# Performance work log

Measured on AMD Instinct MI355X. Metric: run time of the kernel, lower is better.

Reference implementation:

```python
import jax, jax.numpy as jnp
import numpy as np

# static config (matches torch module instantiation)
B, D, NH, HD = 2, 256, 8, 32
NL, NP, DFF = 1, 4, 1024
SHAPES = [(180, 180)]          # (H, W) per level; 180*180 = 32400
STARTS = [0]
LSRC = 32400
N_DET, N_SEG = 200, 100        # SEG_QUERY_NUM=100 -> num_seg_query=300
LQ = N_DET + N_SEG


def _lin(key, dout, din, scale=None):
    scale = scale if scale is not None else 1.0 / np.sqrt(din)
    k1, k2 = jax.random.split(key)
    return (jax.random.normal(k1, (dout, din), jnp.float32) * scale,
            jax.random.normal(k2, (dout,), jnp.float32) * 0.01)


def setup_inputs() -> dict:
    key = jax.random.key(0)
    ks = iter(jax.random.split(key, 64))
    inp = {
        'query': jax.random.normal(next(ks), (B, LQ, D), jnp.float32),
        'query_pos': jax.random.normal(next(ks), (B, LQ, D), jnp.float32),
        'src': jax.random.normal(next(ks), (B, LSRC, D), jnp.float32),
        'pos': jax.random.normal(next(ks), (B, LSRC, D), jnp.float32),
        'reference_points': jax.random.uniform(next(ks), (B, LSRC + LQ, NL, 2), jnp.float32),
        'spatial_shapes': jnp.array(SHAPES, jnp.int32),
        'level_start_index': jnp.array(STARTS, jnp.int32),
    }
    # two MSDeformAttn instances (self_attn = sa_*, cross_attn = ca_*)
    for pre in ('sa', 'ca'):
        inp[pre + '_Wv'], inp[pre + '_bv'] = _lin(next(ks), D, D)
        inp[pre + '_Woff'], inp[pre + '_boff'] = _lin(next(ks), NH * NL * NP * 2, D, scale=0.01)
        inp[pre + '_Waw'], inp[pre + '_baw'] = _lin(next(ks), NH * NL * NP, D, scale=0.01)
        inp[pre + '_Wout'], inp[pre + '_bout'] = _lin(next(ks), D, D)
    for nm in ('norm1', 'norm2', 'normq', 'qa_norm', 'norm3'):
        inp[nm + '_g'] = jnp.ones((D,), jnp.float32)
        inp[nm + '_b'] = jnp.zeros((D,), jnp.float32)
    inp['ffn1_W1'], inp['ffn1_b1'] = _lin(next(ks), DFF, D)
    inp['ffn1_W2'], inp['ffn1_b2'] = _lin(next(ks), D, DFF)
    inp['ffn3_W1'], inp['ffn3_b1'] = _lin(next(ks), DFF, D)
    inp['ffn3_W2'], inp['ffn3_b2'] = _lin(next(ks), D, DFF)
    # TCSLayer: proj(d->2d) then gate1/gate2 (d->d), sigmoid gates
    inp['tcs_Wp'], inp['tcs_bp'] = _lin(next(ks), 2 * D, D)
    inp['tcs_Wg1'], inp['tcs_bg1'] = _lin(next(ks), D, D)
    inp['tcs_Wg2'], inp['tcs_bg2'] = _lin(next(ks), D, D)
    # query self-attention (nn.MultiheadAttention): packed in_proj [3D, D]
    inp['qa_Win'], inp['qa_bin'] = _lin(next(ks), 3 * D, D)
    inp['qa_Wout'], inp['qa_bout'] = _lin(next(ks), D, D)
    return inp


def ln(x, g, b, eps=1e-5):
    m = x.mean(-1, keepdims=True)
    v = ((x - m) ** 2).mean(-1, keepdims=True)
    return (x - m) * jax.lax.rsqrt(v + eps) * g + b


def msda(q, ref, src_v, Wv, bv, Woff, boff, Waw, baw, Wout, bout):
    """MSDeformAttn: value proj -> learned offsets/weights -> bilinear sample -> out proj.
    q [B,Lq,D], ref [B,Lq,NL,2] in [0,1], src_v [B,Lin,D]."""
    Bq, Lq, _ = q.shape
    Lin = src_v.shape[1]
    value = (src_v @ Wv.T + bv).reshape(Bq, Lin, NH, HD).transpose(0, 2, 1, 3)  # [B,NH,Lin,HD]
    off = (q @ Woff.T + boff).reshape(Bq, Lq, NH, NL, NP, 2)
    aw = jax.nn.softmax((q @ Waw.T + baw).reshape(Bq, Lq, NH, NL * NP), -1)
    aw = aw.reshape(Bq, Lq, NH, NL, NP)
    norm = jnp.array([[w, h] for (h, w) in SHAPES], q.dtype)  # [NL,2] = (W,H)
    loc = ref[:, :, None, :, None, :] + off / norm[None, None, None, :, None, :]
    out = jnp.zeros((Bq, NH, Lq, HD), q.dtype)
    for l, (h, w) in enumerate(SHAPES):
        s = STARTS[l]
        v_l = value[:, :, s:s + h * w, :]
        # grid_sample align_corners=False: pixel = loc*size - 0.5, zero padding
        x = loc[:, :, :, l, :, 0] * w - 0.5  # [B,Lq,NH,NP]
        y = loc[:, :, :, l, :, 1] * h - 0.5
        x0 = jnp.floor(x); y0 = jnp.floor(y)
        lx = x - x0; ly = y - y0
        x0i = x0.astype(jnp.int32); y0i = y0.astype(jnp.int32)
        samp = jnp.zeros((Bq, NH, Lq, NP, HD), q.dtype)
        for dy, dx, wgt in ((0, 0, (1 - lx) * (1 - ly)), (0, 1, lx * (1 - ly)),
                            (1, 0, (1 - lx) * ly), (1, 1, lx * ly)):
            xi = x0i + dx; yi = y0i + dy
            valid = ((xi >= 0) & (xi < w) & (yi >= 0) & (yi < h)).astype(q.dtype)
            idx = jnp.clip(yi, 0, h - 1) * w + jnp.clip(xi, 0, w - 1)  # [B,Lq,NH,NP]
            idx_t = idx.transpose(0, 2, 1, 3).reshape(Bq, NH, Lq * NP)
            g = jnp.take_along_axis(v_l, idx_t[..., None], axis=2).reshape(Bq, NH, Lq, NP, HD)
            samp = samp + g * (wgt * valid).transpose(0, 2, 1, 3)[..., None]
        out = out + jnp.einsum('bhqpd,bqhp->bhqd', samp, aw[:, :, :, l, :])
    out = out.transpose(0, 2, 1, 3).reshape(Bq, Lq, NH * HD)
    return out @ Wout.T + bout


def mha(x, pos, Win, bin_, Wout, bout):
    qk = x + pos
    q = (qk @ Win[:D].T + bin_[:D]).reshape(*x.shape[:2], NH, HD)
    k = (qk @ Win[D:2 * D].T + bin_[D:2 * D]).reshape(*x.shape[:2], NH, HD)
    v = (x @ Win[2 * D:].T + bin_[2 * D:]).reshape(*x.shape[:2], NH, HD)
    attn = jax.nn.softmax(jnp.einsum('bqhd,bkhd->bhqk', q, k) / np.sqrt(HD), -1)
    o = jnp.einsum('bhqk,bkhd->bqhd', attn, v).reshape(*x.shape[:2], D)
    return o @ Wout.T + bout


def reference(query, query_pos, src, pos, reference_points, spatial_shapes, level_start_index,
              sa_Wv, sa_bv, sa_Woff, sa_boff, sa_Waw, sa_baw, sa_Wout, sa_bout,
              ca_Wv, ca_bv, ca_Woff, ca_boff, ca_Waw, ca_baw, ca_Wout, ca_bout,
              norm1_g, norm1_b, norm2_g, norm2_b, normq_g, normq_b,
              qa_norm_g, qa_norm_b, norm3_g, norm3_b,
              ffn1_W1, ffn1_b1, ffn1_W2, ffn1_b2,
              ffn3_W1, ffn3_b1, ffn3_W2, ffn3_b2,
              tcs_Wp, tcs_bp, tcs_Wg1, tcs_bg1, tcs_Wg2, tcs_bg2,
              qa_Win, qa_bin, qa_Wout, qa_bout):
    # deformable self-attn over BEV tokens
    src2 = msda(src + pos, reference_points[:, :LSRC], src,
                sa_Wv, sa_bv, sa_Woff, sa_boff, sa_Waw, sa_baw, sa_Wout, sa_bout)
    src = ln(src + src2, norm1_g, norm1_b)
    # FFN 1
    h = jax.nn.relu(src @ ffn1_W1.T + ffn1_b1) @ ffn1_W2.T + ffn1_b2
    src = ln(src + h, norm2_g, norm2_b)
    # TCS gating (USE_SIGMOID_GATE, not SPLIT_GATE, no OCC)
    gd, gs = jnp.split(jax.nn.gelu(src @ tcs_Wp.T + tcs_bp, approximate=False), 2, axis=-1)
    gate_det = jax.nn.sigmoid(gd @ tcs_Wg1.T + tcs_bg1)
    gate_seg = jax.nn.sigmoid(gs @ tcs_Wg2.T + tcs_bg2)
    # gated deformable cross-attn (shared cross_attn weights)
    q_det = msda(query[:, :N_DET] + query_pos[:, :N_DET],
                 reference_points[:, LSRC:LSRC + N_DET], src * gate_det,
                 ca_Wv, ca_bv, ca_Woff, ca_boff, ca_Waw, ca_baw, ca_Wout, ca_bout)
    q_seg = msda(query[:, N_DET:LQ] + query_pos[:, N_DET:LQ],
                 reference_points[:, LSRC + N_DET:LSRC + LQ], src * gate_seg,
                 ca_Wv, ca_bv, ca_Woff, ca_boff, ca_Waw, ca_baw, ca_Wout, ca_bout)
    query2 = jnp.concatenate([q_det, q_seg], 1)
    query = ln(query + query2, normq_g, normq_b)
    # query self-attention (post-norm)
    query = ln(query + mha(query, query_pos, qa_Win, qa_bin, qa_Wout, qa_bout),
               qa_norm_g, qa_norm_b)
    # FFN 3
    h3 = jax.nn.relu(query @ ffn3_W1.T + ffn3_b1) @ ffn3_W2.T + ffn3_b2
    query = ln(query + h3, norm3_g, norm3_b)
    return (query, src, gate_det, gate_seg)
```

## Files before the change

### kernel.cpp

```cpp
#include <hip/hip_runtime.h>
#include <hip/hip_bf16.h>
#include <cmath>

using bf16 = __hip_bfloat16;
typedef __bf16 bf16x8 __attribute__((ext_vector_type(8)));
typedef __bf16 bf16x4 __attribute__((ext_vector_type(4)));
typedef float f32x4 __attribute__((ext_vector_type(4)));

constexpr int D = 256;
constexpr int LSRC = 32400;
constexpr int NB = 2;
constexpr int LQ = 300;
constexpr int NDET = 200;
constexpr int MS = NB * LSRC;
constexpr int MQ = NB * LQ;
constexpr int RP_STRIDE = LSRC + LQ;
constexpr float IMGW = 180.f, IMGH = 180.f;
constexpr int IW = 180, IH = 180;

constexpr long long OFF_Q  = 0;
constexpr long long OFF_S  = (long long)MQ * D;
constexpr long long OFF_GD = OFF_S + (long long)MS * D;
constexpr long long OFF_GS = OFF_GD + (long long)MS * D;

__device__ inline void gload16(const void* g, void* l) {
  __builtin_amdgcn_global_load_lds(
      (const __attribute__((address_space(1))) void*)g,
      (__attribute__((address_space(3))) void*)l, 16, 0, 0);
}

__global__ void detect_kernel(const void* g, int* flag) {
  *flag = (*(const unsigned*)g == 0x3F803F80u) ? 1 : 0;
}

struct CvtEnt { const void* src; void* dst; int n; int f32out; };
struct CvtBatch { CvtEnt e[48]; int blk0[49]; int cnt; };

__global__ __launch_bounds__(256) void cvt_batch_kernel(CvtBatch cb, const int* __restrict__ flag) {
  int bid = blockIdx.x;
  int i = 0;
  for (int j = 1; j < cb.cnt; ++j) if (cb.blk0[j] <= bid) i = j;
  const CvtEnt en = cb.e[i];
  int idx = (bid - cb.blk0[i]) * 2048 + threadIdx.x * 8;
  if (idx >= en.n) return;
  const bool isb = (*flag != 0);
  if (en.f32out) {
    float v[8];
    if (isb) {
      bf16x8 x = *(const bf16x8*)((const __bf16*)en.src + idx);
#pragma unroll
      for (int j = 0; j < 8; ++j) v[j] = (float)x[j];
    } else {
      const float* s = (const float*)en.src + idx;
#pragma unroll
      for (int j = 0; j < 8; ++j) v[j] = s[j];
    }
    float* o = (float*)en.dst + idx;
#pragma unroll
    for (int j = 0; j < 8; ++j) o[j] = v[j];
  } else {
    if (isb) {
      uint4 x = *(const uint4*)((const char*)en.src + (size_t)idx * 2);
      *(uint4*)((char*)en.dst + (size_t)idx * 2) = x;
    } else {
      const float* s = (const float*)en.src + idx;
      bf16x8 o;
#pragma unroll
      for (int j = 0; j < 8; ++j) o[j] = (__bf16)s[j];
      *(bf16x8*)((__bf16*)en.dst + idx) = o;
    }
  }
}

__global__ __launch_bounds__(256) void cvt_add(const void* __restrict__ a, const void* __restrict__ b,
                                               const int* __restrict__ flag,
                                               bf16* __restrict__ a_b, bf16* __restrict__ b_b,
                                               bf16* __restrict__ sum, int n8) {
  int i = blockIdx.x * 256 + threadIdx.x;
  if (i >= n8) return;
  const bool isb = (*flag != 0);
  float va[8], vb[8];
  bf16x8 ab, bb;
  if (isb) {
    ab = *(const bf16x8*)((const __bf16*)a + (size_t)i * 8);
    bb = *(const bf16x8*)((const __bf16*)b + (size_t)i * 8);
#pragma unroll
    for (int j = 0; j < 8; ++j) { va[j] = (float)ab[j]; vb[j] = (float)bb[j]; }
  } else {
    const float* pa = (const float*)a + (size_t)i * 8;
    const float* pb = (const float*)b + (size_t)i * 8;
#pragma unroll
    for (int j = 0; j < 8; ++j) { va[j] = pa[j]; vb[j] = pb[j]; ab[j] = (__bf16)va[j]; bb[j] = (__bf16)vb[j]; }
  }
  bf16x8 sb;
#pragma unroll
  for (int j = 0; j < 8; ++j) sb[j] = (__bf16)(va[j] + vb[j]);
  if (a_b) *(bf16x8*)((__bf16*)a_b + (size_t)i * 8) = ab;
  if (b_b) *(bf16x8*)((__bf16*)b_b + (size_t)i * 8) = bb;
  *(bf16x8*)((__bf16*)sum + (size_t)i * 8) = sb;
}

__global__ __launch_bounds__(256) void add8(const bf16* __restrict__ a, const bf16* __restrict__ b,
                                            bf16* __restrict__ o, int n8) {
  int i = blockIdx.x * 256 + threadIdx.x;
  if (i >= n8) return;
  bf16x8 va = *(const bf16x8*)((const __bf16*)a + (size_t)i * 8);
  bf16x8 vb = *(const bf16x8*)((const __bf16*)b + (size_t)i * 8);
  bf16x8 vo;
#pragma unroll
  for (int j = 0; j < 8; ++j) vo[j] = (__bf16)((float)va[j] + (float)vb[j]);
  *(bf16x8*)((__bf16*)o + (size_t)i * 8) = vo;
}

template<int ACT, int OUTB, int RESM>
__global__ __launch_bounds__(256) void gemm_bt(
    const bf16* __restrict__ A, int lda,
    const bf16* __restrict__ Wt,
    const bf16* __restrict__ bias,
    const void* __restrict__ res,
    void* __restrict__ out, int ldo,
    int M, int N, int K)
{
  __shared__ __bf16 As[64 * 32];
  __shared__ __bf16 Bs[64 * 32];
  const int m0 = blockIdx.x * 64;
  const int n0 = blockIdx.y * 64;
  const int tid = threadIdx.x;
  const int lane = tid & 63, wid = tid >> 6;
  const int wm = (wid >> 1) * 32, wn = (wid & 1) * 32;
  f32x4 acc[2][2] = {};
  const int lr = tid >> 2;
  const int lc = (tid & 3) * 8;
  const bf16* Ap = A + (size_t)(m0 + lr) * lda + lc;
  const bf16* Wp = Wt + (size_t)(n0 + lr) * K + lc;
  __bf16* AsP = &As[8 * tid];
  __bf16* BsP = &Bs[8 * tid];
  const int fr = lane & 15, ks = (lane >> 4) * 8;

  for (int k0 = 0; k0 < K; k0 += 32) {
    __syncthreads();
    gload16((const __bf16*)Ap + k0, AsP);
    gload16((const __bf16*)Wp + k0, BsP);
    __syncthreads();
    bf16x8 a0 = *(const bf16x8*)&As[(wm + fr) * 32 + ks];
    bf16x8 a1 = *(const bf16x8*)&As[(wm + 16 + fr) * 32 + ks];
    bf16x8 b0 = *(const bf16x8*)&Bs[(wn + fr) * 32 + ks];
    bf16x8 b1 = *(const bf16x8*)&Bs[(wn + 16 + fr) * 32 + ks];
    acc[0][0] = __builtin_amdgcn_mfma_f32_16x16x32_bf16(a0, b0, acc[0][0], 0, 0, 0);
    acc[0][1] = __builtin_amdgcn_mfma_f32_16x16x32_bf16(a0, b1, acc[0][1], 0, 0, 0);
    acc[1][0] = __builtin_amdgcn_mfma_f32_16x16x32_bf16(a1, b0, acc[1][0], 0, 0, 0);
    acc[1][1] = __builtin_amdgcn_mfma_f32_16x16x32_bf16(a1, b1, acc[1][1], 0, 0, 0);
  }

  const int rq = (lane >> 4) * 4;
#pragma unroll
  for (int fm = 0; fm < 2; ++fm)
#pragma unroll
  for (int fn = 0; fn < 2; ++fn) {
    int ncol = n0 + wn + fn * 16 + fr;
    if (ncol >= N) continue;
    float bvs = (float)bias[ncol];
#pragma unroll
    for (int i = 0; i < 4; ++i) {
      int mrow = m0 + wm + fm * 16 + rq + i;
      if (mrow >= M) continue;
      float v = acc[fm][fn][i] + bvs;
      if (RESM == 1) v += (float)((const bf16*)res)[(size_t)mrow * ldo + ncol];
      else if (RESM == 2) v += ((const float*)res)[(size_t)mrow * ldo + ncol];
      if (ACT == 1) v = fmaxf(v, 0.f);
      else if (ACT == 2) v = 0.5f * v * (1.f + erff(v * 0.7071067811865476f));
      else if (ACT == 3) v = 1.f / (1.f + __expf(-v));
      if (OUTB) ((bf16*)out)[(size_t)mrow * ldo + ncol] = (bf16)v;
      else ((float*)out)[(size_t)mrow * ldo + ncol] = v;
    }
  }
}

template<int ACT, int OUTB, int RESM, int EMIT>
__global__ __launch_bounds__(256) void gemm128(
    const bf16* __restrict__ A, int lda,
    const bf16* __restrict__ Wt,
    const bf16* __restrict__ bias,
    const void* __restrict__ res,
    void* __restrict__ out, int ldo,
    int M, int N, int K,
    const int* __restrict__ flagp, void* __restrict__ ob, long long eoff)
{
  __shared__ __bf16 As[128 * 32];
  __shared__ __bf16 Bs[128 * 32];
  const int m0 = blockIdx.x * 128;
  const int n0 = blockIdx.y * 128;
  const int tid = threadIdx.x;
  const int lane = tid & 63, wid = tid >> 6;
  const int wr = (wid >> 1) * 64, wc = (wid & 1) * 64;
  const int fr = lane & 15, ks = (lane >> 4) * 8;
  f32x4 acc[4][4] = {};

  const int srow = tid >> 2;
  const int scol = (tid & 3) * 8;
  const bf16* Ap0 = A + (size_t)(m0 + srow) * lda + scol;
  const bf16* Ap1 = A + (size_t)(m0 + 64 + srow) * lda + scol;
  const bf16* Bp0 = Wt + (size_t)(n0 + srow) * K + scol;
  const bf16* Bp1 = Wt + (size_t)(n0 + 64 + srow) * K + scol;
  __bf16* AsP0 = &As[8 * tid];
  __bf16* AsP1 = &As[64 * 32 + 8 * tid];
  __bf16* BsP0 = &Bs[8 * tid];
  __bf16* BsP1 = &Bs[64 * 32 + 8 * tid];

  for (int k0 = 0; k0 < K; k0 += 32) {
    __syncthreads();
    gload16((const __bf16*)Ap0 + k0, AsP0);
    gload16((const __bf16*)Ap1 + k0, AsP1);
    gload16((const __bf16*)Bp0 + k0, BsP0);
    gload16((const __bf16*)Bp1 + k0, BsP1);
    __syncthreads();
    bf16x8 af[4], bfv[4];
#pragma unroll
    for (int m = 0; m < 4; ++m) af[m]  = *(const bf16x8*)&As[(wr + m * 16 + fr) * 32 + ks];
#pragma unroll
    for (int n = 0; n < 4; ++n) bfv[n] = *(const bf16x8*)&Bs[(wc + n * 16 + fr) * 32 + ks];
#pragma unroll
    for (int m = 0; m < 4; ++m)
#pragma unroll
      for (int n = 0; n < 4; ++n)
        acc[m][n] = __builtin_amdgcn_mfma_f32_16x16x32_bf16(af[m], bfv[n], acc[m][n], 0, 0, 0);
  }

  const bool isb = EMIT ? (*flagp != 0) : false;
  const int rq = (lane >> 4) * 4;
#pragma unroll
  for (int m = 0; m < 4; ++m) {
    const int mb = m0 + wr + m * 16 + rq;
#pragma unroll
    for (int n = 0; n < 4; ++n) {
      const int ncol = n0 + wc + n * 16 + fr;
      const float bvs = (float)bias[ncol];
#pragma unroll
      for (int i = 0; i < 4; ++i) {
        const int mrow = mb + i;
        if (mrow >= M) continue;
        float v = acc[m][n][i] + bvs;
        if (RESM == 1) v += (float)((const bf16*)res)[(size_t)mrow * ldo + ncol];
        else if (RESM == 2) v += ((const float*)res)[(size_t)mrow * ldo + ncol];
        if (ACT == 1) v = fmaxf(v, 0.f);
        else if (ACT == 2) v = 0.5f * v * (1.f + erff(v * 0.7071067811865476f));
        else if (ACT == 3) v = 1.f / (1.f + __expf(-v));
        if (OUTB) ((bf16*)out)[(size_t)mrow * ldo + ncol] = (bf16)v;
        else ((float*)out)[(size_t)mrow * ldo + ncol] = v;
        if (EMIT) {
          long long eo = eoff + (long long)mrow * ldo + ncol;
          if (isb) ((__bf16*)ob)[eo] = (__bf16)v;
          else ((float*)ob)[eo] = v;
        }
      }
    }
  }
}

__global__ __launch_bounds__(256) void gemm_gated(
    const bf16* __restrict__ S, const bf16* __restrict__ G, int lda,
    const bf16* __restrict__ Wt,
    const bf16* __restrict__ bias,
    bf16* __restrict__ out, int ldo,
    int M, int N, int K)
{
  __shared__ __bf16 As[128 * 32];
  __shared__ __bf16 Bs[128 * 32];
  const int m0 = blockIdx.x * 128;
  const int n0 = blockIdx.y * 128;
  const int tid = threadIdx.x;
  const int lane = tid & 63, wid = tid >> 6;
  const int wr = (wid >> 1) * 64, wc = (wid & 1) * 64;
  const int fr = lane & 15, ks = (lane >> 4) * 8;
  f32x4 acc[4][4] = {};

  const int srow = tid >> 2;
  const int scol = (tid & 3) * 8;
  const bf16* Sp0 = S + (size_t)(m0 + srow) * lda + scol;
  const bf16* Sp1 = S + (size_t)(m0 + 64 + srow) * lda + scol;
  const bf16* Gp0 = G + (size_t)(m0 + srow) * lda + scol;
  const bf16* Gp1 = G + (size_t)(m0 + 64 + srow) * lda + scol;
  const bf16* Bp0 = Wt + (size_t)(n0 + srow) * K + scol;
  const bf16* Bp1 = Wt + (size_t)(n0 + 64 + srow) * K + scol;
  __bf16* AsP0 = &As[8 * tid];
  __bf16* AsP1 = &As[64 * 32 + 8 * tid];

  for (int k0 = 0; k0 < K; k0 += 32) {
    bf16x8 s0 = *(const bf16x8*)((const __bf16*)Sp0 + k0);
    bf16x8 g0 = *(const bf16x8*)((const __bf16*)Gp0 + k0);
    bf16x8 s1 = *(const bf16x8*)((const __bf16*)Sp1 + k0);
    bf16x8 g1 = *(const bf16x8*)((const __bf16*)Gp1 + k0);
    bf16x8 a0, a1;
#pragma unroll
    for (int j = 0; j < 8; ++j) {
      a0[j] = (__bf16)((float)s0[j] * (float)g0[j]);
      a1[j] = (__bf16)((float)s1[j] * (float)g1[j]);
    }
    __syncthreads();
    *(bf16x8*)AsP0 = a0;
    *(bf16x8*)AsP1 = a1;
    gload16((const __bf16*)Bp0 + k0, &Bs[8 * tid]);
    gload16((const __bf16*)Bp1 + k0, &Bs[64 * 32 + 8 * tid]);
    __syncthreads();
    bf16x8 af[4], bfv[4];
#pragma unroll
    for (int m = 0; m < 4; ++m) af[m]  = *(const bf16x8*)&As[(wr + m * 16 + fr) * 32 + ks];
#pragma unroll
    for (int n = 0; n < 4; ++n) bfv[n] = *(const bf16x8*)&Bs[(wc + n * 16 + fr) * 32 + ks];
#pragma unroll
    for (int m = 0; m < 4; ++m)
#pragma unroll
      for (int n = 0; n < 4; ++n)
        acc[m][n] = __builtin_amdgcn_mfma_f32_16x16x32_bf16(af[m], bfv[n], acc[m][n], 0, 0, 0);
  }

  const int rq = (lane >> 4) * 4;
#pragma unroll
  for (int m = 0; m < 4; ++m) {
    const int mb = m0 + wr + m * 16 + rq;
#pragma unroll
    for (int n = 0; n < 4; ++n) {
      const int ncol = n0 + wc + n * 16 + fr;
      const float bvs = (float)bias[ncol];
#pragma unroll
      for (int i = 0; i < 4; ++i) {
        const int mrow = mb + i;
        if (mrow >= M) continue;
        out[(size_t)mrow * ldo + ncol] = (bf16)(acc[m][n][i] + bvs);
      }
    }
  }
}

template<int RESM, int EMIT, int OUTF>
__global__ __launch_bounds__(256) void gemm_ln(
    const bf16* __restrict__ A, int lda,
    const bf16* __restrict__ Wt,
    const bf16* __restrict__ bias,
    const void* __restrict__ res,
    const bf16* __restrict__ g, const bf16* __restrict__ b,
    bf16* __restrict__ outb, float* __restrict__ outf,
    int M, int K,
    const int* __restrict__ flagp, void* __restrict__ ob, long long eoff)
{
  __shared__ __bf16 As[64 * 32];
  __shared__ __bf16 Bs[256 * 32];
  __shared__ float redS[4][64], redQ[4][64];
  const int m0 = blockIdx.x * 64;
  const int tid = threadIdx.x, lane = tid & 63, wid = tid >> 6;
  const int wc = wid * 64;
  const int fr = lane & 15, ks = (lane >> 4) * 8;
  f32x4 acc[4][4] = {};
  const int srow = tid >> 2, scol = (tid & 3) * 8;
  const bf16* Ap = A + (size_t)(m0 + srow) * lda + scol;
  const bf16* Bp = Wt + (size_t)srow * K + scol;

  for (int k0 = 0; k0 < K; k0 += 32) {
    __syncthreads();
    gload16((const __bf16*)Ap + k0, &As[8 * tid]);
#pragma unroll
    for (int j = 0; j < 4; ++j)
      gload16((const __bf16*)(Bp + (size_t)j * 64 * K) + k0, &Bs[j * 64 * 32 + 8 * tid]);
    __syncthreads();
    bf16x8 af[4], bfv[4];
#pragma unroll
    for (int m = 0; m < 4; ++m) af[m]  = *(const bf16x8*)&As[(m * 16 + fr) * 32 + ks];
#pragma unroll
    for (int n = 0; n < 4; ++n) bfv[n] = *(const bf16x8*)&Bs[(wc + n * 16 + fr) * 32 + ks];
#pragma unroll
    for (int m = 0; m < 4; ++m)
#pragma unroll
      for (int n = 0; n < 4; ++n)
        acc[m][n] = __builtin_amdgcn_mfma_f32_16x16x32_bf16(af[m], bfv[n], acc[m][n], 0, 0, 0);
  }

  const int rq = (lane >> 4) * 4;
  float bvals[4], gvals[4], bb2[4];
#pragma unroll
  for (int n = 0; n < 4; ++n) {
    bvals[n] = (float)bias[wc + n * 16 + fr];
    gvals[n] = (float)g[wc + n * 16 + fr];
    bb2[n]   = (float)b[wc + n * 16 + fr];
  }
#pragma unroll
  for (int m = 0; m < 4; ++m)
#pragma unroll
  for (int i = 0; i < 4; ++i) {
    const int mrow = m0 + m * 16 + rq + i;
#pragma unroll
    for (int n = 0; n < 4; ++n) {
      float r;
      if (RESM == 1) r = (float)((const bf16*)res)[(size_t)mrow * 256 + wc + n * 16 + fr];
      else           r = ((const float*)res)[(size_t)mrow * 256 + wc + n * 16 + fr];
      acc[m][n][i] += bvals[n] + r;
    }
    float s = acc[m][0][i] + acc[m][1][i] + acc[m][2][i] + acc[m][3][i];
    float q = acc[m][0][i] * acc[m][0][i] + acc[m][1][i] * acc[m][1][i]
            + acc[m][2][i] * acc[m][2][i] + acc[m][3][i] * acc[m][3][i];
#pragma unroll
    for (int off = 1; off <= 8; off <<= 1) {
      s += __shfl_xor(s, off);
      q += __shfl_xor(q, off);
    }
    if (fr == 0) { redS[wid][m * 16 + rq + i] = s; redQ[wid][m * 16 + rq + i] = q; }
  }
  __syncthreads();
  const bool isb = EMIT ? (*flagp != 0) : false;
#pragma unroll
  for (int m = 0; m < 4; ++m)
#pragma unroll
  for (int i = 0; i < 4; ++i) {
    const int rl = m * 16 + rq + i;
    const int mrow = m0 + rl;
    if (mrow >= M) continue;
    float ts = redS[0][rl] + redS[1][rl] + redS[2][rl] + redS[3][rl];
    float tq = redQ[0][rl] + redQ[1][rl] + redQ[2][rl] + redQ[3][rl];
    float mean = ts * (1.f / 256.f);
    float var = tq * (1.f / 256.f) - mean * mean;
    float rstd = rsqrtf(var + 1e-5f);
#pragma unroll
    for (int n = 0; n < 4; ++n) {
      const int col = wc + n * 16 + fr;
      float y = (acc[m][n][i] - mean) * rstd * gvals[n] + bb2[n];
      if (outb) outb[(size_t)mrow * 256 + col] = (bf16)y;
      if (OUTF) outf[(size_t)mrow * 256 + col] = y;
      if (EMIT) {
        long long eo = eoff + (long long)mrow * 256 + col;
        if (isb) ((__bf16*)ob)[eo] = (__bf16)y;
        else ((float*)ob)[eo] = y;
      }
    }
  }
}

__global__ __launch_bounds__(256) void msda_sample4(
    const float* __restrict__ oa,
    const float* __restrict__ rpf, int rp_base, int qi0, int qcnt4, int lqrow,
    const bf16* __restrict__ val, bf16* __restrict__ out) {
  int blk = blockIdx.x;
  int b = blk / qcnt4;
  int wid = threadIdx.x >> 6, lane = threadIdx.x & 63;
  int qi = qi0 + (blk % qcnt4) * 4 + wid;
  size_t row = (size_t)b * lqrow + qi;
  int h = lane >> 3, d0 = (lane & 7) * 4;
  const __bf16* vb = (const __bf16*)val + (size_t)b * LSRC * 256 + h * 32 + d0;
  float rx = rpf[((size_t)b * RP_STRIDE + rp_base + qi) * 2 + 0];
  float ry = rpf[((size_t)b * RP_STRIDE + rp_base + qi) * 2 + 1];
  const float* offp = oa + row * 96 + h * 8;
  const float* awp  = oa + row * 96 + 64 + h * 4;
  float a0 = awp[0], a1 = awp[1], a2 = awp[2], a3 = awp[3];
  float mx = fmaxf(fmaxf(a0, a1), fmaxf(a2, a3));
  float e0 = __expf(a0 - mx), e1 = __expf(a1 - mx), e2 = __expf(a2 - mx), e3 = __expf(a3 - mx);
  float rs = 1.f / (e0 + e1 + e2 + e3);
  float aws[4] = { e0 * rs, e1 * rs, e2 * rs, e3 * rs };
  float o0 = 0.f, o1 = 0.f, o2 = 0.f, o3 = 0.f;
#pragma unroll
  for (int p = 0; p < 4; ++p) {
    float x = rx * IMGW + offp[p * 2 + 0] - 0.5f;
    float y = ry * IMGH + offp[p * 2 + 1] - 0.5f;
    float x0f = floorf(x), y0f = floorf(y);
    float lx = x - x0f, ly = y - y0f;
    int x0 = (int)x0f, y0 = (int)y0f;
#pragma unroll
    for (int dy = 0; dy < 2; ++dy)
#pragma unroll
    for (int dx = 0; dx < 2; ++dx) {
      int xi = x0 + dx, yi = y0 + dy;
      if (xi >= 0 && xi < IW && yi >= 0 && yi < IH) {
        float wgt = aws[p] * (dx ? lx : 1.f - lx) * (dy ? ly : 1.f - ly);
        bf16x4 gv = *(const bf16x4*)(vb + (size_t)(yi * IW + xi) * 256);
        o0 += wgt * (float)gv[0]; o1 += wgt * (float)gv[1];
        o2 += wgt * (float)gv[2]; o3 += wgt * (float)gv[3];
      }
    }
  }
  bf16x4 ov;
  ov[0] = (__bf16)o0; ov[1] = (__bf16)o1; ov[2] = (__bf16)o2; ov[3] = (__bf16)o3;
  *(bf16x4*)((__bf16*)out + row * 256 + h * 32 + d0) = ov;
}

__global__ __launch_bounds__(256) void mha_attn(
    const float* __restrict__ qk,
    const float* __restrict__ v,
    bf16* __restrict__ o) {
  __shared__ float probs[4][304];
  int bh = blockIdx.x / 75;
  int j  = blockIdx.x % 75;
  int b = bh >> 3, h = bh & 7;
  int wid = threadIdx.x >> 6, lane = threadIdx.x & 63;
  const float scale = 0.17677669529663687f;
  int q = j * 4 + wid;
  const float* qv = qk + ((size_t)(b * 300 + q)) * 512 + h * 32;
  float p[5];
  float mx = -1e30f;
#pragma unroll
  for (int s5 = 0; s5 < 5; ++s5) {
    int k = lane + 64 * s5;
    float sacc = -1e30f;
    if (k < 300) {
      const float* kv = qk + ((size_t)(b * 300 + k)) * 512 + 256 + h * 32;
      float sd = 0.f;
#pragma unroll
      for (int dd = 0; dd < 32; ++dd) sd += qv[dd] * kv[dd];
      sacc = sd * scale;
    }
    p[s5] = sacc;
    mx = fmaxf(mx, sacc);
  }
#pragma unroll
  for (int off = 32; off; off >>= 1) mx = fmaxf(mx, __shfl_xor(mx, off));
  float ssum = 0.f;
#pragma unroll
  for (int s5 = 0; s5 < 5; ++s5) {
    p[s5] = (p[s5] > -1e29f) ? __expf(p[s5] - mx) : 0.f;
    ssum += p[s5];
  }
#pragma unroll
  for (int off = 32; off; off >>= 1) ssum += __shfl_xor(ssum, off);
  float rinv = 1.f / ssum;
#pragma unroll
  for (int s5 = 0; s5 < 5; ++s5) {
    int k = lane + 64 * s5;
    if (k < 300) probs[wid][k] = p[s5] * rinv;
  }
  __syncthreads();
  {
    int d = lane & 31, half = lane >> 5;
    float acc = 0.f;
    for (int k = half * 150; k < half * 150 + 150; ++k)
      acc += probs[wid][k] * v[((size_t)(b * 300 + k)) * 256 + h * 32 + d];
    acc += __shfl_xor(acc, 32);
    if (lane < 32) o[((size_t)(b * 300 + q)) * 256 + h * 32 + d] = (bf16)acc;
  }
}

extern "C" void kernel_launch(void* const* d_in, const int* in_sizes, int n_in,
                              void* d_out, int out_size, void* d_ws, size_t ws_size,
                              hipStream_t stream) {
  (void)n_in; (void)out_size; (void)ws_size;
  const size_t SZ = (size_t)MS * D * sizeof(bf16);

  char* w = (char*)d_ws;
  auto carve = [&](size_t bytes) { char* p = w; w += (bytes + 255) & ~(size_t)255; return p; };

  int*   flag = (int*)carve(256);
  float* rp_f = (float*)carve((size_t)NB * RP_STRIDE * 2 * 4);

  bf16* wb[51] = {};
  bf16* wcat_s = nullptr; bf16* bcat_s = nullptr;
  bf16* wcat_q = nullptr; bf16* bcat_q = nullptr;
  for (int i = 7; i <= 50; ++i) {
    if (i == 9)       { wcat_s = (bf16*)carve((size_t)96 * 256 * 2); wb[9]  = wcat_s; }
    else if (i == 10) { bcat_s = (bf16*)carve(96 * 2);               wb[10] = bcat_s; }
    else if (i == 11) { wb[11] = wcat_s + 64 * 256; }
    else if (i == 12) { wb[12] = bcat_s + 64; }
    else if (i == 17) { wcat_q = (bf16*)carve((size_t)96 * 256 * 2); wb[17] = wcat_q; }
    else if (i == 18) { bcat_q = (bf16*)carve(96 * 2);               wb[18] = bcat_q; }
    else if (i == 19) { wb[19] = wcat_q + 64 * 256; }
    else if (i == 20) { wb[20] = bcat_q + 64; }
    else wb[i] = (bf16*)carve((size_t)in_sizes[i] * 2);
  }

  bf16* query_b     = (bf16*)carve((size_t)MQ * D * 2);
  bf16* query_pos_b = (bf16*)carve((size_t)MQ * D * 2);
  bf16* qx_q        = (bf16*)carve((size_t)MQ * D * 2);
  bf16* att_q       = (bf16*)carve((size_t)MQ * D * 2);
  bf16* q_x         = (bf16*)carve((size_t)MQ * D * 2);
  bf16* qpx         = (bf16*)carve((size_t)MQ * D * 2);
  bf16* mha_o       = (bf16*)carve((size_t)MQ * D * 2);
  bf16* lnq_b       = (bf16*)carve((size_t)MQ * D * 2);
  bf16* qh          = (bf16*)carve((size_t)MQ * 1024 * 2);
  float* qoffawb    = (float*)carve((size_t)MQ * 96 * 4);
  float* q_res      = (float*)carve((size_t)MQ * D * 4);
  float* qk_f       = (float*)carve((size_t)MQ * 512 * 4);
  float* v_f        = (float*)carve((size_t)MQ * D * 4);

  char* A = carve(SZ);
  char* B = carve(SZ);
  char* C = carve(SZ);
  char* Dd = carve(SZ);
  char* E = carve(SZ);
  carve(512 * 1024);

  const bf16* query     = (const bf16*)d_in[0];
  const bf16* query_pos = (const bf16*)d_in[1];
  const bf16* src       = (const bf16*)d_in[2];
  const bf16* pos       = (const bf16*)d_in[3];

  dim3 blk(256);
  const int GS64  = (MS + 63) / 64;
  const int GQ64  = (MQ + 63) / 64;
  const int G128  = (MS + 127) / 128;
  const int G128h = (MS / 2 + 127) / 128;

  detect_kernel<<<1, 1, 0, stream>>>(d_in[23], flag);
  {
    CvtBatch cb{};
    int nb = 0, cnt = 0;
    auto addcvt = [&](const void* s, void* dst, int n, int f32o) {
      cb.e[cnt] = { s, dst, n, f32o };
      cb.blk0[cnt] = nb;
      nb += (n + 2047) / 2048;
      ++cnt;
    };
    addcvt(d_in[4], rp_f, in_sizes[4], 1);
    for (int i = 7; i <= 50; ++i) addcvt(d_in[i], wb[i], in_sizes[i], 0);
    cb.cnt = cnt;
    cvt_batch_kernel<<<nb, blk, 0, stream>>>(cb, flag);
  }
  bf16* src_b = (bf16*)A;
  bf16* qx    = (bf16*)C;
  cvt_add<<<MS * D / 8 / 256, blk, 0, stream>>>(src, pos, flag, src_b, nullptr, qx, MS * D / 8);
  cvt_add<<<MQ * D / 8 / 256, blk, 0, stream>>>(query, query_pos, flag, query_b, query_pos_b, qx_q, MQ * D / 8);

  float* offawb = (float*)B;
  bf16*  val    = (bf16*)Dd;
  gemm_bt<0,0,0><<<dim3(GS64,2), blk, 0, stream>>>(qx, 256, wb[9], wb[10], nullptr, offawb, 96, MS, 96, 256);
  gemm128<0,1,0,0><<<dim3(G128,2), blk, 0, stream>>>(src_b, 256, wb[7], wb[8], nullptr, val, 256, MS, 256, 256, nullptr, nullptr, 0);
  bf16* samp = (bf16*)C;
  msda_sample4<<<NB * (LSRC / 4), blk, 0, stream>>>(offawb, rp_f, 0, 0, LSRC / 4, LSRC, val, samp);
  bf16* lnx = (bf16*)C;
  gemm_ln<1,0,0><<<GS64, blk, 0, stream>>>(samp, 256, wb[13], wb[14], src_b, wb[23], wb[24],
                                           lnx, nullptr, MS, 256, nullptr, nullptr, 0);

  bf16* srcout = (bf16*)A;
  {
    const int CH = MS / 2;
    const int GC128 = (CH + 127) / 128;
    const int GC64  = (CH + 63) / 64;
    bf16* hid = (bf16*)Dd;
    for (int c = 0; c < 2; ++c) {
      size_t ro = (size_t)c * CH * 256;
      gemm128<1,1,0,0><<<dim3(GC128,8), blk, 0, stream>>>(lnx + ro, 256, wb[33], wb[34], nullptr, hid, 1024, CH, 1024, 256, nullptr, nullptr, 0);
      gemm_ln<1,1,0><<<GC64, blk, 0, stream>>>(hid, 1024, wb[35], wb[36], lnx + ro, wb[25], wb[26],
                                               srcout + ro, nullptr, CH, 1024, flag, d_out, OFF_S + (long long)ro);
    }
  }

  bf16* gdt = (bf16*)B;
  bf16* gst = (bf16*)E;
  {
    const int CH = MS / 2;
    bf16* proj = (bf16*)C;
    for (int c = 0; c < 2; ++c) {
      size_t ro = (size_t)c * CH * 256;
      gemm128<2,1,0,0><<<dim3(G128h,4), blk, 0, stream>>>(srcout + ro, 256, wb[41], wb[42], nullptr, proj, 512, CH, 512, 256, nullptr, nullptr, 0);
      gemm128<3,1,0,1><<<dim3(G128h,2), blk, 0, stream>>>(proj,       512, wb[43], wb[44], nullptr, gdt + ro, 256, CH, 256, 256, flag, d_out, OFF_GD + (long long)ro);
      gemm128<3,1,0,1><<<dim3(G128h,2), blk, 0, stream>>>(proj + 256, 512, wb[45], wb[46], nullptr, gst + ro, 256, CH, 256, 256, flag, d_out, OFF_GS + (long long)ro);
    }
  }

  gemm_bt<0,0,0><<<dim3(GQ64,2), blk, 0, stream>>>(qx_q, 256, wb[17], wb[18], nullptr, qoffawb, 96, MQ, 96, 256);

  gemm_gated<<<dim3(G128,2), blk, 0, stream>>>(srcout, gdt, 256, wb[15], wb[16], val, 256, MS, 256, 256);
  msda_sample4<<<NB * (NDET / 4), blk, 0, stream>>>(qoffawb, rp_f, LSRC, 0, NDET / 4, LQ, val, att_q);
  gemm_gated<<<dim3(G128,2), blk, 0, stream>>>(srcout, gst, 256, wb[15], wb[16], val, 256, MS, 256, 256);
  msda_sample4<<<NB * ((LQ - NDET) / 4), blk, 0, stream>>>(qoffawb, rp_f, LSRC, NDET, (LQ - NDET) / 4, LQ, val, att_q);

  gemm_ln<1,0,1><<<GQ64, blk, 0, stream>>>(att_q, 256, wb[21], wb[22], query_b, wb[27], wb[28],
                                           q_x, q_res, MQ, 256, nullptr, nullptr, 0);

  add8<<<MQ * D / 8 / 256, blk, 0, stream>>>(q_x, query_pos_b, qpx, MQ * D / 8);
  gemm_bt<0,0,0><<<dim3(GQ64,8), blk, 0, stream>>>(qpx, 256, wb[47], wb[48], nullptr, qk_f, 512, MQ, 512, 256);
  gemm_bt<0,0,0><<<dim3(GQ64,4), blk, 0, stream>>>(q_x, 256, wb[47] + (size_t)512 * 256, wb[48] + 512, nullptr, v_f, 256, MQ, 256, 256);
  mha_attn<<<NB * 8 * 75, blk, 0, stream>>>(qk_f, v_f, mha_o);
  gemm_ln<2,0,1><<<GQ64, blk, 0, stream>>>(mha_o, 256, wb[49], wb[50], q_res, wb[29], wb[30],
                                           q_x, q_res, MQ, 256, nullptr, nullptr, 0);

  gemm_bt<1,1,0><<<dim3(GQ64,16), blk, 0, stream>>>(q_x, 256, wb[37], wb[38], nullptr, qh, 1024, MQ, 1024, 256);
  gemm_ln<2,1,0><<<GQ64, blk, 0, stream>>>(qh, 1024, wb[39], wb[40], q_res, wb[31], wb[32],
                                           lnq_b, nullptr, MQ, 1024, flag, d_out, OFF_Q);
}
```

Before: 822.1 us.

## Double K-step per barrier and add XCD-aware block swizzle to GEMMs

Each GEMM kernel now loads two 32-wide K slices into separate LDS buffers per iteration and runs both MFMA groups before the next barrier. This halves the number of __syncthreads and lets more global loads be in flight at once. A block-index swizzle also groups consecutive tiles onto the same XCD for better L2 locality. The cost is doubled LDS use per block, which may reduce occupancy.

```diff
diff --git a/kernel.cpp b/kernel.cpp
--- a/kernel.cpp
+++ b/kernel.cpp
@@ -27,6 +27,12 @@
   __builtin_amdgcn_global_load_lds(
       (const __attribute__((address_space(1))) void*)g,
       (__attribute__((address_space(3))) void*)l, 16, 0, 0);
+}
+
+__device__ inline int xcd_swz(int b, int nwg) {
+  int q = nwg >> 3, r = nwg & 7;
+  int xcd = b & 7, i = b >> 3;
+  return (xcd < r ? xcd * (q + 1) : r * (q + 1) + (xcd - r) * q) + i;
 }
 
 __global__ void detect_kernel(const void* g, int* flag) {
@@ -121,10 +127,13 @@
     void* __restrict__ out, int ldo,
     int M, int N, int K)
 {
-  __shared__ __bf16 As[64 * 32];
-  __shared__ __bf16 Bs[64 * 32];
-  const int m0 = blockIdx.x * 64;
-  const int n0 = blockIdx.y * 64;
+  __shared__ __bf16 As[2][64 * 32];
+  __shared__ __bf16 Bs[2][64 * 32];
+  const int gy = gridDim.y;
+  const int nwg = gridDim.x * gy;
+  const int t = xcd_swz(blockIdx.y * gridDim.x + blockIdx.x, nwg);
+  const int m0 = (t / gy) * 64;
+  const int n0 = (t % gy) * 64;
   const int tid = threadIdx.x;
   const int lane = tid & 63, wid = tid >> 6;
   const int wm = (wid >> 1) * 32, wn = (wid & 1) * 32;
@@ -133,23 +142,28 @@
   const int lc = (tid & 3) * 8;
   const bf16* Ap = A + (size_t)(m0 + lr) * lda + lc;
   const bf16* Wp = Wt + (size_t)(n0 + lr) * K + lc;
-  __bf16* AsP = &As[8 * tid];
-  __bf16* BsP = &Bs[8 * tid];
   const int fr = lane & 15, ks = (lane >> 4) * 8;
 
-  for (int k0 = 0; k0 < K; k0 += 32) {
+  for (int k0 = 0; k0 < K; k0 += 64) {
     __syncthreads();
-    gload16((const __bf16*)Ap + k0, AsP);
-    gload16((const __bf16*)Wp + k0, BsP);
+#pragma unroll
+    for (int kk = 0; kk < 2; ++kk) {
+      const int kc = k0 + kk * 32;
+      gload16((const __bf16*)Ap + kc, &As[kk][8 * tid]);
+      gload16((const __bf16*)Wp + kc, &Bs[kk][8 * tid]);
+    }
     __syncthreads();
-    bf16x8 a0 = *(const bf16x8*)&As[(wm + fr) * 32 + ks];
-    bf16x8 a1 = *(const bf16x8*)&As[(wm + 16 + fr) * 32 + ks];
-    bf16x8 b0 = *(const bf16x8*)&Bs[(wn + fr) * 32 + ks];
-    bf16x8 b1 = *(const bf16x8*)&Bs[(wn + 16 + fr) * 32 + ks];
-    acc[0][0] = __builtin_amdgcn_mfma_f32_16x16x32_bf16(a0, b0, acc[0][0], 0, 0, 0);
-    acc[0][1] = __builtin_amdgcn_mfma_f32_16x16x32_bf16(a0, b1, acc[0][1], 0, 0, 0);
-    acc[1][0] = __builtin_amdgcn_mfma_f32_16x16x32_bf16(a1, b0, acc[1][0], 0, 0, 0);
-    acc[1][1] = __builtin_amdgcn_mfma_f32_16x16x32_bf16(a1, b1, acc[1][1], 0, 0, 0);
+#pragma unroll
+    for (int kk = 0; kk < 2; ++kk) {
+      bf16x8 a0 = *(const bf16x8*)&As[kk][(wm + fr) * 32 + ks];
+      bf16x8 a1 = *(const bf16x8*)&As[kk][(wm + 16 + fr) * 32 + ks];
+      bf16x8 b0 = *(const bf16x8*)&Bs[kk][(wn + fr) * 32 + ks];
+      bf16x8 b1 = *(const bf16x8*)&Bs[kk][(wn + 16 + fr) * 32 + ks];
+      acc[0][0] = __builtin_amdgcn_mfma_f32_16x16x32_bf16(a0, b0, acc[0][0], 0, 0, 0);
+      acc[0][1] = __builtin_amdgcn_mfma_f32_16x16x32_bf16(a0, b1, acc[0][1], 0, 0, 0);
+      acc[1][0] = __builtin_amdgcn_mfma_f32_16x16x32_bf16(a1, b0, acc[1][0], 0, 0, 0);
+      acc[1][1] = __builtin_amdgcn_mfma_f32_16x16x32_bf16(a1, b1, acc[1][1], 0, 0, 0);
+    }
   }
 
   const int rq = (lane >> 4) * 4;
@@ -186,10 +200,13 @@
     int M, int N, int K,
     const int* __restrict__ flagp, void* __restrict__ ob, long long eoff)
 {
-  __shared__ __bf16 As[128 * 32];
-  __shared__ __bf16 Bs[128 * 32];
-  const int m0 = blockIdx.x * 128;
-  const int n0 = blockIdx.y * 128;
+  __shared__ __bf16 As[2][128 * 32];
+  __shared__ __bf16 Bs[2][128 * 32];
+  const int gy = gridDim.y;
+  const int nwg = gridDim.x * gy;
+  const int t = xcd_swz(blockIdx.y * gridDim.x + blockIdx.x, nwg);
+  const int m0 = (t / gy) * 128;
+  const int n0 = (t % gy) * 128;
   const int tid = threadIdx.x;
   const int lane = tid & 63, wid = tid >> 6;
   const int wr = (wid >> 1) * 64, wc = (wid & 1) * 64;
@@ -202,28 +219,31 @@
   const bf16* Ap1 = A + (size_t)(m0 + 64 + srow) * lda + scol;
   const bf16* Bp0 = Wt + (size_t)(n0 + srow) * K + scol;
   const bf16* Bp1 = Wt + (size_t)(n0 + 64 + srow) * K + scol;
-  __bf16* AsP0 = &As[8 * tid];
-  __bf16* AsP1 = &As[64 * 32 + 8 * tid];
-  __bf16* BsP0 = &Bs[8 * tid];
-  __bf16* BsP1 = &Bs[64 * 32 + 8 * tid];
-
-  for (int k0 = 0; k0 < K; k0 += 32) {
+
+  for (int k0 = 0; k0 < K; k0 += 64) {
     __syncthreads();
-    gload16((const __bf16*)Ap0 + k0, AsP0);
-    gload16((const __bf16*)Ap1 + k0, AsP1);
-    gload16((const __bf16*)Bp0 + k0, BsP0);
-    gload16((const __bf16*)Bp1 + k0, BsP1);
+#pragma unroll
+    for (int kk = 0; kk < 2; ++kk) {
+      const int kc = k0 + kk * 32;
+      gload16((const __bf16*)Ap0 + kc, &As[kk][8 * tid]);
+      gload16((const __bf16*)Ap1 + kc, &As[kk][64 * 32 + 8 * tid]);
+      gload16((const __bf16*)Bp0 + kc, &Bs[kk][8 * tid]);
+      gload16((const __bf16*)Bp1 + kc, &Bs[kk][64 * 32 + 8 * tid]);
+    }
     __syncthreads();
-    bf16x8 af[4], bfv[4];
-#pragma unroll
-    for (int m = 0; m < 4; ++m) af[m]  = *(const bf16x8*)&As[(wr + m * 16 + fr) * 32 + ks];
-#pragma unroll
-    for (int n = 0; n < 4; ++n) bfv[n] = *(const bf16x8*)&Bs[(wc + n * 16 + fr) * 32 + ks];
-#pragma unroll
-    for (int m = 0; m < 4; ++m)
-#pragma unroll
-      for (int n = 0; n < 4; ++n)
-        acc[m][n] = __builtin_amdgcn_mfma_f32_16x16x32_bf16(af[m], bfv[n], acc[m][n], 0, 0, 0);
+#pragma unroll
+    for (int kk = 0; kk < 2; ++kk) {
+      bf16x8 af[4], bfv[4];
+#pragma unroll
+      for (int m = 0; m < 4; ++m) af[m]  = *(const bf16x8*)&As[kk][(wr + m * 16 + fr) * 32 + ks];
+#pragma unroll
+      for (int n = 0; n < 4; ++n) bfv[n] = *(const bf16x8*)&Bs[kk][(wc + n * 16 + fr) * 32 + ks];
+#pragma unroll
+      for (int m = 0; m < 4; ++m)
+#pragma unroll
+        for (int n = 0; n < 4; ++n)
+          acc[m][n] = __builtin_amdgcn_mfma_f32_16x16x32_bf16(af[m], bfv[n], acc[m][n], 0, 0, 0);
+    }
   }
 
   const bool isb = EMIT ? (*flagp != 0) : false;
@@ -264,10 +284,13 @@
     bf16* __restrict__ out, int ldo,
     int M, int N, int K)
 {
-  __shared__ __bf16 As[128 * 32];
-  __shared__ __bf16 Bs[128 * 32];
-  const int m0 = blockIdx.x * 128;
-  const int n0 = blockIdx.y * 128;
+  __shared__ __bf16 As[2][128 * 32];
+  __shared__ __bf16 Bs[2][128 * 32];
+  const int gy = gridDim.y;
+  const int nwg = gridDim.x * gy;
+  const int t = xcd_swz(blockIdx.y * gridDim.x + blockIdx.x, nwg);
+  const int m0 = (t / gy) * 128;
+  const int n0 = (t % gy) * 128;
   const int tid = threadIdx.x;
   const int lane = tid & 63, wid = tid >> 6;
   const int wr = (wid >> 1) * 64, wc = (wid & 1) * 64;
@@ -282,36 +305,45 @@
   const bf16* Gp1 = G + (size_t)(m0 + 64 + srow) * lda + scol;
   const bf16* Bp0 = Wt + (size_t)(n0 + srow) * K + scol;
   const bf16* Bp1 = Wt + (size_t)(n0 + 64 + srow) * K + scol;
-  __bf16* AsP0 = &As[8 * tid];
-  __bf16* AsP1 = &As[64 * 32 + 8 * tid];
-
-  for (int k0 = 0; k0 < K; k0 += 32) {
-    bf16x8 s0 = *(const bf16x8*)((const __bf16*)Sp0 + k0);
-    bf16x8 g0 = *(const bf16x8*)((const __bf16*)Gp0 + k0);
-    bf16x8 s1 = *(const bf16x8*)((const __bf16*)Sp1 + k0);
-    bf16x8 g1 = *(const bf16x8*)((const __bf16*)Gp1 + k0);
-    bf16x8 a0, a1;
-#pragma unroll
-    for (int j = 0; j < 8; ++j) {
-      a0[j] = (__bf16)((float)s0[j] * (float)g0[j]);
-      a1[j] = (__bf16)((float)s1[j] * (float)g1[j]);
+
+  for (int k0 = 0; k0 < K; k0 += 64) {
+    bf16x8 a0[2], a1[2];
+#pragma unroll
+    for (int kk = 0; kk < 2; ++kk) {
+      const int kc = k0 + kk * 32;
+      bf16x8 s0 = *(const bf16x8*)((const __bf16*)Sp0 + kc);
+      bf16x8 g0 = *(const bf16x8*)((const __bf16*)Gp0 + kc);
+      bf16x8 s1 = *(const bf16x8*)((const __bf16*)Sp1 + kc);
+      bf16x8 g1 = *(const bf16x8*)((const __bf16*)Gp1 + kc);
+#pragma unroll
+      for (int j = 0; j < 8; ++j) {
+        a0[kk][j] = (__bf16)((float)s0[j] * (float)g0[j]);
+        a1[kk][j] = (__bf16)((float)s1[j] * (float)g1[j]);
+      }
     }
     __syncthreads();
-    *(bf16x8*)AsP0 = a0;
-    *(bf16x8*)AsP1 = a1;
-    gload16((const __bf16*)Bp0 + k0, &Bs[8 * tid]);
-    gload16((const __bf16*)Bp1 + k0, &Bs[64 * 32 + 8 * tid]);
+#pragma unroll
+    for (int kk = 0; kk < 2; ++kk) {
+      const int kc = k0 + kk * 32;
+      *(bf16x8*)&As[kk][8 * tid] = a0[kk];
+      *(bf16x8*)&As[kk][64 * 32 + 8 * tid] = a1[kk];
+      gload16((const __bf16*)Bp0 + kc, &Bs[kk][8 * tid]);
+      gload16((const __bf16*)Bp1 + kc, &Bs[kk][64 * 32 + 8 * tid]);
+    }
     __syncthreads();
-    bf16x8 af[4], bfv[4];
-#pragma unroll
-    for (int m = 0; m < 4; ++m) af[m]  = *(const bf16x8*)&As[(wr + m * 16 + fr) * 32 + ks];
-#pragma unroll
-    for (int n = 0; n < 4; ++n) bfv[n] = *(const bf16x8*)&Bs[(wc + n * 16 + fr) * 32 + ks];
-#pragma unroll
-    for (int m = 0; m < 4; ++m)
-#pragma unroll
-      for (int n = 0; n < 4; ++n)
-        acc[m][n] = __builtin_amdgcn_mfma_f32_16x16x32_bf16(af[m], bfv[n], acc[m][n], 0, 0, 0);
+#pragma unroll
+    for (int kk = 0; kk < 2; ++kk) {
+      bf16x8 af[4], bfv[4];
+#pragma unroll
+      for (int m = 0; m < 4; ++m) af[m]  = *(const bf16x8*)&As[kk][(wr + m * 16 + fr) * 32 + ks];
+#pragma unroll
+      for (int n = 0; n < 4; ++n) bfv[n] = *(const bf16x8*)&Bs[kk][(wc + n * 16 + fr) * 32 + ks];
+#pragma unroll
+      for (int m = 0; m < 4; ++m)
+#pragma unroll
+        for (int n = 0; n < 4; ++n)
+          acc[m][n] = __builtin_amdgcn_mfma_f32_16x16x32_bf16(af[m], bfv[n], acc[m][n], 0, 0, 0);
+    }
   }
 
   const int rq = (lane >> 4) * 4;
@@ -343,8 +375,8 @@
     int M, int K,
     const int* __restrict__ flagp, void* __restrict__ ob, long long eoff)
 {
-  __shared__ __bf16 As[64 * 32];
-  __shared__ __bf16 Bs[256 * 32];
+  __shared__ __bf16 As[2][64 * 32];
+  __shared__ __bf16 Bs[2][256 * 32];
   __shared__ float redS[4][64], redQ[4][64];
   const int m0 = blockIdx.x * 64;
   const int tid = threadIdx.x, lane = tid & 63, wid = tid >> 6;
@@ -355,23 +387,30 @@
   const bf16* Ap = A + (size_t)(m0 + srow) * lda + scol;
   const bf16* Bp = Wt + (size_t)srow * K + scol;
 
-  for (int k0 = 0; k0 < K; k0 += 32) {
+  for (int k0 = 0; k0 < K; k0 += 64) {
     __syncthreads();
-    gload16((const __bf16*)Ap + k0, &As[8 * tid]);
-#pragma unroll
-    for (int j = 0; j < 4; ++j)
-      gload16((const __bf16*)(Bp + (size_t)j * 64 * K) + k0, &Bs[j * 64 * 32 + 8 * tid]);
+#pragma unroll
+    for (int kk = 0; kk < 2; ++kk) {
+      const int kc = k0 + kk * 32;
+      gload16((const __bf16*)Ap + kc, &As[kk][8 * tid]);
+#pragma unroll
+      for (int j = 0; j < 4; ++j)
+        gload16((const __bf16*)(Bp + (size_t)j * 64 * K) + kc, &Bs[kk][j * 64 * 32 + 8 * tid]);
+    }
     __syncthreads();
-    bf16x8 af[4], bfv[4];
-#pragma unroll
-    for (int m = 0; m < 4; ++m) af[m]  = *(const bf16x8*)&As[(m * 16 + fr) * 32 + ks];
-#pragma unroll
-    for (int n = 0; n < 4; ++n) bfv[n] = *(const bf16x8*)&Bs[(wc + n * 16 + fr) * 32 + ks];
-#pragma unroll
-    for (int m = 0; m < 4; ++m)
-#pragma unroll
-      for (int n = 0; n < 4; ++n)
-        acc[m][n] = __builtin_amdgcn_mfma_f32_16x16x32_bf16(af[m], bfv[n], acc[m][n], 0, 0, 0);
+#pragma unroll
+    for (int kk = 0; kk < 2; ++kk) {
+      bf16x8 af[4], bfv[4];
+#pragma unroll
+      for (int m = 0; m < 4; ++m) af[m]  = *(const bf16x8*)&As[kk][(m * 16 + fr) * 32 + ks];
+#pragma unroll
+      for (int n = 0; n < 4; ++n) bfv[n] = *(const bf16x8*)&Bs[kk][(wc + n * 16 + fr) * 32 + ks];
+#pragma unroll
+      for (int m = 0; m < 4; ++m)
+#pragma unroll
+        for (int n = 0; n < 4; ++n)
+          acc[m][n] = __builtin_amdgcn_mfma_f32_16x16x32_bf16(af[m], bfv[n], acc[m][n], 0, 0, 0);
+    }
   }
 
   const int rq = (lane >> 4) * 4;
```

New measurement: 756.3 us. -8.0%, faster.
